# Optimization experiments

Hardware: AMD Instinct MI355X
Metric: run time of the kernel (lower is better)

Reference implementation:

```python
import jax, jax.numpy as jnp
import numpy as np
import math

N_LAYERS = 2
N_HEADS = 8
D_MODEL = 512
D_FF = 2048
B = 2
L = 2048
GELU_C = 0.7978845608028654  # sqrt(2/pi)
LN_EPS = 1e-5


def gelu_tanh(x):
    # faithful to the module's custom GELU: 0.5*x*(1+tanh(sqrt(2/pi)*(x+0.044715*x^3)))
    return 0.5 * x * (1.0 + jnp.tanh(GELU_C * (x + 0.044715 * x * x * x)))


def layernorm(x, g, b):
    m = jnp.mean(x, axis=-1, keepdims=True)
    v = jnp.mean((x - m) ** 2, axis=-1, keepdims=True)
    return (x - m) * jax.lax.rsqrt(v + LN_EPS) * g + b


def setup_inputs() -> dict:
    key = jax.random.key(0)
    ks = jax.random.split(key, 24)
    w = lambda k, shape: jax.random.normal(k, shape, dtype=jnp.float32) * 0.02
    inp = {
        "x": jax.random.normal(ks[0], (B, L, D_MODEL), dtype=jnp.float32),
        # tau is exp(tau_learner(...)) in the full model -> positive scalar per batch
        "tau": jax.random.uniform(ks[1], (B, 1), dtype=jnp.float32) + 0.5,
        "delta": jax.random.normal(ks[2], (B, L), dtype=jnp.float32) * 0.1,
        # NStransformer builds an upper-triangular causal mask (True = masked)
        "att_mask": jnp.triu(jnp.ones((L, L), dtype=bool), k=1),
        "Wq": w(ks[3], (N_LAYERS, D_MODEL, D_MODEL)), "bq": jnp.zeros((N_LAYERS, D_MODEL), jnp.float32),
        "Wk": w(ks[4], (N_LAYERS, D_MODEL, D_MODEL)), "bk": jnp.zeros((N_LAYERS, D_MODEL), jnp.float32),
        "Wv": w(ks[5], (N_LAYERS, D_MODEL, D_MODEL)), "bv": jnp.zeros((N_LAYERS, D_MODEL), jnp.float32),
        "Wo": w(ks[6], (N_LAYERS, D_MODEL, D_MODEL)), "bo": jnp.zeros((N_LAYERS, D_MODEL), jnp.float32),
        # conv1/conv2 are kernel_size=1 Conv1d == pointwise linears
        "W1": w(ks[7], (N_LAYERS, D_MODEL, D_FF)), "b1": jnp.zeros((N_LAYERS, D_FF), jnp.float32),
        "W2": w(ks[8], (N_LAYERS, D_FF, D_MODEL)), "b2": jnp.zeros((N_LAYERS, D_MODEL), jnp.float32),
        "ln1_g": jnp.ones((N_LAYERS, D_MODEL), jnp.float32), "ln1_b": jnp.zeros((N_LAYERS, D_MODEL), jnp.float32),
        "ln2_g": jnp.ones((N_LAYERS, D_MODEL), jnp.float32), "ln2_b": jnp.zeros((N_LAYERS, D_MODEL), jnp.float32),
        "lnf_g": jnp.ones((D_MODEL,), jnp.float32), "lnf_b": jnp.zeros((D_MODEL,), jnp.float32),
    }
    return inp


def reference(x, tau, delta, att_mask, Wq, bq, Wk, bk, Wv, bv, Wo, bo,
              W1, b1, W2, b2, ln1_g, ln1_b, ln2_g, ln2_b, lnf_g, lnf_b):
    Bsz, Ls, D = x.shape
    H = N_HEADS
    E = D // H
    scale = 1.0 / math.sqrt(E)
    t = tau[:, None, None, :]    # (B,1) -> (B,1,1,1)
    d = delta[:, None, None, :]  # (B,L) -> (B,1,1,L)
    neg_inf = jnp.float32(-jnp.inf)
    for l in range(N_LAYERS):
        q = (x @ Wq[l] + bq[l]).reshape(Bsz, Ls, H, E)
        k = (x @ Wk[l] + bk[l]).reshape(Bsz, Ls, H, E)
        v = (x @ Wv[l] + bv[l]).reshape(Bsz, Ls, H, E)
        # de-stationary scores: QK^T * tau + delta, then masked softmax
        scores = jnp.einsum('blhe,bshe->bhls', q, k) * t + d  # (B,H,L,S)
        scores = jnp.where(att_mask, neg_inf, scores)
        A = jax.nn.softmax(scale * scores, axis=-1)  # dropout is identity in eval
        V = jnp.einsum('bhls,bshd->blhd', A, v).reshape(Bsz, Ls, D)
        x = (V @ Wo[l] + bo[l]) + x
        xb = layernorm(x, ln1_g[l], ln1_b[l])
        h = gelu_tanh(xb @ W1[l] + b1[l])   # conv1 (k=1)
        o = h @ W2[l] + b2[l]               # conv2 (k=1)
        x = layernorm(o + xb, ln2_g[l], ln2_b[l])
    return layernorm(x, lnf_g, lnf_b)
```

## Files before the change

### kernel.cpp

```cpp
#include <hip/hip_runtime.h>
#include <stdint.h>

#define DM   512
#define DFF  2048
#define NH   8
#define EH   64
#define SEQ  2048
#define NBAT 2
#define NTOK (NBAT*SEQ)
#define LOG2E 1.44269504088896340736f

typedef __attribute__((ext_vector_type(8))) short  s16x8;
typedef __attribute__((ext_vector_type(8))) __bf16 bf16x8;
typedef __attribute__((ext_vector_type(4))) float  f32x4;

__device__ __forceinline__ short f2bf(float f) {
  union { float f; unsigned int i; } c; c.f = f;
  unsigned int x = c.i;
  x += 0x7fffu + ((x >> 16) & 1u);
  return (short)(x >> 16);
}
__device__ __forceinline__ float bf2f(short u) {
  union { unsigned int i; float f; } c;
  c.i = ((unsigned int)(unsigned short)u) << 16;
  return c.f;
}
__device__ __forceinline__ f32x4 mfma16(bf16x8 a, bf16x8 b, f32x4 c) {
  return __builtin_amdgcn_mfma_f32_16x16x32_bf16(a, b, c, 0, 0, 0);
}
__device__ __forceinline__ void gl_lds16(const short* g, short* l) {
  __builtin_amdgcn_global_load_lds(
      (const __attribute__((address_space(1))) unsigned int*)(const void*)g,
      (__attribute__((address_space(3))) unsigned int*)(void*)l, 16, 0, 0);
}

__global__ __launch_bounds__(256) void fill_code_f32(float* __restrict__ out,
                                                     float code)
{
  out[blockIdx.x * 256 + threadIdx.x] = code;
}

__global__ __launch_bounds__(256) void prep_all(
    const float* __restrict__ Wq, const float* __restrict__ Wk,
    const float* __restrict__ Wv, const float* __restrict__ Wo,
    const float* __restrict__ W1, const float* __restrict__ W2,
    short* __restrict__ Wqkvt, short* __restrict__ Wot,
    short* __restrict__ W1t,   short* __restrict__ W2t,
    const float* __restrict__ x, float* __restrict__ sumf,
    short* __restrict__ x16)
{
  if (blockIdx.x >= 3072) {
    int i = (blockIdx.x - 3072) * 256 + threadIdx.x;
    float v = x[i];
    sumf[i] = v;
    x16[i]  = f2bf(v);
    return;
  }
  int gw   = blockIdx.x * 4 + (threadIdx.x >> 6);
  int lane = threadIdx.x & 63;
  int l = gw / 6144;
  int g = gw % 6144;
  const float* src; short* dst; int K, N, gi;
  if (g < 2048) {
    int w = g >> 9; gi = g & 511; K = 512; N = 512;
    src = (w == 0 ? Wq : w == 1 ? Wk : w == 2 ? Wv : Wo) + l * 262144;
    dst = (w < 3) ? (Wqkvt + l * 786432 + w * 262144) : (Wot + l * 262144);
  } else if (g < 4096) {
    gi = g - 2048; K = 512; N = 2048;
    src = W1 + l * 1048576; dst = W1t + l * 1048576;
  } else {
    gi = g - 4096; K = 2048; N = 512;
    src = W2 + l * 1048576; dst = W2t + l * 1048576;
  }
  int nb = N >> 6;
  int n  = (gi % nb) * 64 + lane;
  int k0 = (gi / nb) * 8;
  s16x8 v;
  #pragma unroll
  for (int i = 0; i < 8; i++) v[i] = f2bf(src[(size_t)(k0 + i) * N + n]);
  *(s16x8*)(dst + (size_t)n * K + k0) = v;
}

__global__ __launch_bounds__(256) void skred_ln(
    const short* __restrict__ parts, const float* __restrict__ bias,
    const float* __restrict__ rf, const short* __restrict__ rb,
    const float* __restrict__ g, const float* __restrict__ bb,
    float* __restrict__ sumf, short* __restrict__ outb, int mode)
{
  const int row  = blockIdx.x * 4 + (threadIdx.x >> 6);
  const int lane = threadIdx.x & 63;
  const int col  = lane * 8;
  const size_t base = (size_t)row * DM + col;
  float t[8];
  #pragma unroll
  for (int j = 0; j < 8; j++) t[j] = bias[col + j];
  #pragma unroll
  for (int p = 0; p < 4; p++) {
    s16x8 v = *(const s16x8*)(parts + (size_t)p * (NTOK * DM) + base);
    #pragma unroll
    for (int j = 0; j < 8; j++) t[j] += bf2f(v[j]);
  }
  if (mode == 0) {
    #pragma unroll
    for (int j = 0; j < 8; j++) t[j] += rf[base + j];
  } else {
    s16x8 v = *(const s16x8*)(rb + base);
    #pragma unroll
    for (int j = 0; j < 8; j++) t[j] += bf2f(v[j]);
  }
  float s = 0.f, ss = 0.f;
  #pragma unroll
  for (int j = 0; j < 8; j++) { s += t[j]; ss += t[j] * t[j]; }
  #pragma unroll
  for (int off = 32; off > 0; off >>= 1) {
    s += __shfl_xor(s, off); ss += __shfl_xor(ss, off);
  }
  float mean = s * (1.f / DM);
  float var  = ss * (1.f / DM) - mean * mean;
  float rstd = rsqrtf(var + 1e-5f);
  if (mode == 0) {
    #pragma unroll
    for (int j = 0; j < 8; j++) {
      sumf[base + j] = t[j];
      outb[base + j] = f2bf((t[j] - mean) * rstd * g[col + j] + bb[col + j]);
    }
  } else {
    #pragma unroll
    for (int j = 0; j < 8; j++) {
      float y = (t[j] - mean) * rstd * g[col + j] + bb[col + j];
      sumf[base + j] = y;
      outb[base + j] = f2bf(y);
    }
  }
}

template<int TM>
__global__ __launch_bounds__(256) void gemm_bt(
    const short* __restrict__ A, const short* __restrict__ Bt,
    int M, int N, int K, int KS, int mode,
    const float* __restrict__ bq, const float* __restrict__ bk,
    const float* __restrict__ bv,
    short* __restrict__ oq, short* __restrict__ okk, short* __restrict__ ov)
{
  __shared__ short As[2][2][TM * 32];
  __shared__ short Bs[2][2][128 * 32];
  constexpr int MT = TM / 32;
  const int tid  = threadIdx.x;
  const int lane = tid & 63;
  const int wid  = tid >> 6;
  const int lm   = lane & 15, quad = lane >> 4;
  const int nbn  = N >> 7;
  const int nb2  = (M / TM) * nbn;
  const int ks   = blockIdx.x / nb2;
  const int rem  = blockIdx.x % nb2;
  const int m0   = (rem / nbn) * TM;
  const int n0   = (rem % nbn) << 7;
  const int wm   = (wid & 1) * (TM / 2), wn = (wid >> 1) * 64;
  const int Kc   = K / KS;
  const int kbeg = ks * Kc;

  f32x4 acc[MT][4];
  #pragma unroll
  for (int i = 0; i < MT; i++)
    #pragma unroll
    for (int j = 0; j < 4; j++) acc[i][j] = (f32x4){0.f, 0.f, 0.f, 0.f};

  const short* Abase = A  + (size_t)m0 * K;
  const short* Bbase = Bt + (size_t)n0 * K;

  auto stage = [&](int b_, int k0) {
    #pragma unroll
    for (int half = 0; half < 2; half++) {
      const int kk = k0 + half * 32;
      #pragma unroll
      for (int j = 0; j < TM / 64; j++) {
        int c = j * 256 + wid * 64 + lane;
        gl_lds16(Abase + (size_t)(c >> 2) * K + kk + (c & 3) * 8,
                 &As[b_][half][(j * 256 + wid * 64) * 8]);
      }
      #pragma unroll
      for (int j = 0; j < 2; j++) {
        int c = j * 256 + wid * 64 + lane;
        gl_lds16(Bbase + (size_t)(c >> 2) * K + kk + (c & 3) * 8,
                 &Bs[b_][half][(j * 256 + wid * 64) * 8]);
      }
    }
  };

  stage(0, kbeg);
  int buf = 0;
  for (int k0 = kbeg; k0 < kbeg + Kc; k0 += 64) {
    __syncthreads();
    if (k0 + 64 < kbeg + Kc) stage(buf ^ 1, k0 + 64);
    #pragma unroll
    for (int half = 0; half < 2; half++) {
      bf16x8 af[MT], bfr[4];
      #pragma unroll
      for (int t = 0; t < MT; t++)
        af[t] = *(const bf16x8*)
            &As[buf][half][(wm + t * 16 + lm) * 32 + quad * 8];
      #pragma unroll
      for (int t = 0; t < 4; t++)
        bfr[t] = *(const bf16x8*)
            &Bs[buf][half][(wn + t * 16 + lm) * 32 + quad * 8];
      #pragma unroll
      for (int mt = 0; mt < MT; mt++)
        #pragma unroll
        for (int nt = 0; nt < 4; nt++)
          acc[mt][nt] = mfma16(af[mt], bfr[nt], acc[mt][nt]);
    }
    buf ^= 1;
  }

  #pragma unroll
  for (int mt = 0; mt < MT; mt++) {
    int row = m0 + wm + mt * 16 + quad * 4;
    #pragma unroll
    for (int nt = 0; nt < 4; nt++) {
      int col = n0 + wn + nt * 16 + lm;
      f32x4 v = acc[mt][nt];
      if (mode == 0) {
        int which = col >> 9; int d = col & 511;
        int hh = d >> 6; int e = d & 63;
        const float* bias = which == 0 ? bq : which == 1 ? bk : bv;
        float bb = bias[d];
        #pragma unroll
        for (int r = 0; r < 4; r++) {
          int tok = row + r; int bI = tok >> 11, li = tok & 2047;
          float val = v[r] + bb;
          if (which == 0)
            oq [(((size_t)bI * NH + hh) * SEQ + li) * EH + e] = f2bf(val);
          else if (which == 1)
            okk[(((size_t)bI * NH + hh) * SEQ + li) * EH + e] = f2bf(val);
          else
            ov [(((size_t)bI * NH + hh) * EH + e) * SEQ + li] = f2bf(val);
        }
      } else if (mode == 2) {
        float bb = bq[col];
        #pragma unroll
        for (int r = 0; r < 4; r++) {
          float x = v[r] + bb;
          float u = 0.7978845608f * (x + 0.044715f * x * x * x);
          float t = 1.f - 2.f / (1.f + __expf(2.f * u));
          size_t idx = (size_t)(row + r) * N + col;
          oq[idx] = f2bf(0.5f * x * (1.f + t));
        }
      } else {
        short* op = oq + (size_t)ks * M * N;
        #pragma unroll
        for (int r = 0; r < 4; r++)
          op[(size_t)(row + r) * N + col] = f2bf(v[r]);
      }
    }
  }
}

__global__ __launch_bounds__(256) void attn_v7(
    const short* __restrict__ Q, const short* __restrict__ Kg,
    const short* __restrict__ Vt,
    const float* __restrict__ tau, const float* __restrict__ delta,
    short* __restrict__ opart, float* __restrict__ lpart)
{
  __shared__ short Ks[64 * 72];
  __shared__ short Vs[64 * 72];
  __shared__ short Ps[4][16 * 72];
  const int tid  = threadIdx.x;
  const int lane = tid & 63, wid = tid >> 6;
  const int lm = lane & 15, quad = lane >> 4;
  const int t    = blockIdx.x >> 2;
  const int part = blockIdx.x & 3;
  const int qb = 31 - (t & 31);
  const int h  = (t >> 5) & 7;
  const int b  = t >> 8;
  const int q0 = qb * 64;
  const int qw = q0 + wid * 16;
  const size_t bhq = ((size_t)b * NH + h) * SEQ;
  const short* kbase = Kg + bhq * EH;
  const short* vbase = Vt + ((size_t)b * NH + h) * (size_t)(EH * SEQ);

  const int nblk = qb + 1;
  const int kb0 = (nblk * part) >> 2;
  const int kb1 = (nblk * (part + 1)) >> 2;

  bf16x8 qf0 = *(const bf16x8*)(Q + (bhq + qw + lm) * EH + quad * 8);
  bf16x8 qf1 = *(const bf16x8*)(Q + (bhq + qw + lm) * EH + 32 + quad * 8);

  const float st2 = 0.125f * LOG2E * tau[b];
  f32x4 O[4];
  #pragma unroll
  for (int i = 0; i < 4; i++) O[i] = (f32x4){0.f, 0.f, 0.f, 0.f};
  float lr[4] = {0.f, 0.f, 0.f, 0.f};

  const int c0 = tid, c1 = tid + 256;
  const int r0 = c0 >> 3, ch0 = (c0 & 7) * 8;
  const int r1 = c1 >> 3, ch1 = (c1 & 7) * 8;

  for (int kb = kb0; kb < kb1; kb++) {
    const int s0 = kb << 6;
    s16x8 ka = *(const s16x8*)(kbase + (size_t)(s0 + r0) * EH + ch0);
    s16x8 kb_ = *(const s16x8*)(kbase + (size_t)(s0 + r1) * EH + ch1);
    s16x8 va = *(const s16x8*)(vbase + (size_t)r0 * SEQ + s0 + ch0);
    s16x8 vb = *(const s16x8*)(vbase + (size_t)r1 * SEQ + s0 + ch1);
    __syncthreads();
    *(s16x8*)&Ks[r0 * 72 + ch0] = ka;
    *(s16x8*)&Ks[r1 * 72 + ch1] = kb_;
    *(s16x8*)&Vs[r0 * 72 + ch0] = va;
    *(s16x8*)&Vs[r1 * 72 + ch1] = vb;
    __syncthreads();

    f32x4 S[4];
    #pragma unroll
    for (int nt = 0; nt < 4; nt++) {
      S[nt] = (f32x4){0.f, 0.f, 0.f, 0.f};
      S[nt] = mfma16(qf0, *(const bf16x8*)&Ks[(nt*16 + lm) * 72 + quad * 8], S[nt]);
      S[nt] = mfma16(qf1, *(const bf16x8*)&Ks[(nt*16 + lm) * 72 + 32 + quad * 8], S[nt]);
    }
    float dl[4];
    #pragma unroll
    for (int nt = 0; nt < 4; nt++)
      dl[nt] = fmaf(0.125f * LOG2E, delta[(size_t)b * SEQ + s0 + nt * 16 + lm],
                    -8.f);

    const bool diag = (kb == qb);
    #pragma unroll
    for (int r = 0; r < 4; r++) {
      float sc[4];
      #pragma unroll
      for (int nt = 0; nt < 4; nt++) sc[nt] = fmaf(st2, S[nt][r], dl[nt]);
      if (diag) {
        int rowq = qw + quad * 4 + r;
        #pragma unroll
        for (int nt = 0; nt < 4; nt++)
          if (s0 + nt * 16 + lm > rowq) sc[nt] = -__builtin_inff();
      }
      unsigned int u0 = __float_as_uint(exp2f(sc[0]));
      unsigned int u1 = __float_as_uint(exp2f(sc[1]));
      unsigned int u2 = __float_as_uint(exp2f(sc[2]));
      unsigned int u3 = __float_as_uint(exp2f(sc[3]));
      lr[r] += (__uint_as_float(u0 & 0xffff0000u) +
                __uint_as_float(u1 & 0xffff0000u)) +
               (__uint_as_float(u2 & 0xffff0000u) +
                __uint_as_float(u3 & 0xffff0000u));
      short* pr = &Ps[wid][(quad * 4 + r) * 72];
      pr[lm]      = (short)(u0 >> 16);
      pr[16 + lm] = (short)(u1 >> 16);
      pr[32 + lm] = (short)(u2 >> 16);
      pr[48 + lm] = (short)(u3 >> 16);
    }

    bf16x8 pf0 = *(const bf16x8*)&Ps[wid][lm * 72 + quad * 8];
    bf16x8 pf1 = *(const bf16x8*)&Ps[wid][lm * 72 + 32 + quad * 8];
    #pragma unroll
    for (int et = 0; et < 4; et++) {
      O[et] = mfma16(pf0, *(const bf16x8*)&Vs[(et*16 + lm) * 72 + quad * 8], O[et]);
      O[et] = mfma16(pf1, *(const bf16x8*)&Vs[(et*16 + lm) * 72 + 32 + quad * 8], O[et]);
    }
  }

  #pragma unroll
  for (int r = 0; r < 4; r++) {
    float s = lr[r];
    #pragma unroll
    for (int off = 1; off < 16; off <<= 1) s += __shfl_xor(s, off);
    lr[r] = s;
  }

  const int slot = ((t << 2) | part);
  short* ob = opart + (size_t)slot * 4096;
  float* lb = lpart + (size_t)slot * 64;
  #pragma unroll
  for (int r = 0; r < 4; r++) {
    int qloc = wid * 16 + quad * 4 + r;
    #pragma unroll
    for (int et = 0; et < 4; et++)
      ob[qloc * 64 + et * 16 + lm] = f2bf(O[et][r]);
    if (lm == 0) lb[qloc] = lr[r];
  }
}

__global__ __launch_bounds__(256) void attn_reduce(
    const short* __restrict__ opart, const float* __restrict__ lpart,
    short* __restrict__ Oa)
{
  const int t = blockIdx.x;
  const int qb = 31 - (t & 31);
  const int h  = (t >> 5) & 7;
  const int b  = t >> 8;
  const int q0 = qb * 64;
  #pragma unroll
  for (int i = 0; i < 16; i++) {
    int idx = i * 256 + threadIdx.x;
    int q = idx >> 6, e = idx & 63;
    float l = 0.f, o = 0.f;
    #pragma unroll
    for (int p = 0; p < 4; p++) {
      int slot = t * 4 + p;
      l += lpart[(size_t)slot * 64 + q];
      o += bf2f(opart[(size_t)slot * 4096 + idx]);
    }
    Oa[((size_t)b * SEQ + q0 + q) * DM + h * EH + e] = f2bf(o / l);
  }
}

__global__ __launch_bounds__(256) void ln_kernel(
    const float* in, const float* __restrict__ g, const float* __restrict__ bb,
    float* outf, short* outb)
{
  int row  = blockIdx.x * 4 + (threadIdx.x >> 6);
  int lane = threadIdx.x & 63;
  const float* p = in + (size_t)row * DM;
  float v[8]; float s = 0.f, ss = 0.f;
  #pragma unroll
  for (int i = 0; i < 8; i++) {
    float x = p[lane + i * 64]; v[i] = x; s += x; ss += x * x;
  }
  #pragma unroll
  for (int off = 32; off > 0; off >>= 1) {
    s += __shfl_xor(s, off); ss += __shfl_xor(ss, off);
  }
  float mean = s * (1.f / DM);
  float var  = ss * (1.f / DM) - mean * mean;
  float rstd = rsqrtf(var + 1e-5f);
  #pragma unroll
  for (int i = 0; i < 8; i++) {
    int c = lane + i * 64;
    float y = (v[i] - mean) * rstd * g[c] + bb[c];
    if (outf) outf[(size_t)row * DM + c] = y;
    if (outb) outb[(size_t)row * DM + c] = f2bf(y);
  }
}

extern "C" void kernel_launch(void* const* d_in, const int* in_sizes, int n_in,
                              void* d_out, int out_size, void* d_ws, size_t ws_size,
                              hipStream_t stream)
{
  float* out = (float*)d_out;

  if (ws_size < (size_t)62918656) {
    fill_code_f32<<<2097152 / 256, 256, 0, stream>>>(
        out, 1200.f + (float)(ws_size >> 20));
    return;
  }

  const float* x    = (const float*)d_in[0];
  const float* tau  = (const float*)d_in[1];
  const float* del  = (const float*)d_in[2];
  const float* Wq = (const float*)d_in[4];
  const float* bq = (const float*)d_in[5];
  const float* Wk = (const float*)d_in[6];
  const float* bk = (const float*)d_in[7];
  const float* Wv = (const float*)d_in[8];
  const float* bv = (const float*)d_in[9];
  const float* Wo = (const float*)d_in[10];
  const float* bo = (const float*)d_in[11];
  const float* W1 = (const float*)d_in[12];
  const float* b1 = (const float*)d_in[13];
  const float* W2 = (const float*)d_in[14];
  const float* b2 = (const float*)d_in[15];
  const float* ln1g = (const float*)d_in[16];
  const float* ln1b = (const float*)d_in[17];
  const float* ln2g = (const float*)d_in[18];
  const float* ln2b = (const float*)d_in[19];
  const float* lnfg = (const float*)d_in[20];
  const float* lnfb = (const float*)d_in[21];

  char* ws = (char*)d_ws;
  float* sumf  = (float*)(ws + 0);
  short* x16   = (short*)(ws + 8388608);
  short* xb16  = (short*)(ws + 12582912);
  short* q16   = (short*)(ws + 16777216);
  short* k16   = (short*)(ws + 20971520);
  short* vt16  = (short*)(ws + 25165824);
  short* at16  = (short*)(ws + 29360128);
  short* h16   = (short*)(ws + 33554432);
  short* Wqkvt = (short*)(ws + 50331648);
  short* Wot   = (short*)(ws + 53477376);
  short* W1t   = (short*)(ws + 54525952);
  short* W2t   = (short*)(ws + 58720256);
  short* aopart = (short*)(ws + 33554432);
  float* alpart = (float*)(ws + 12582912);
  short* oppart = (short*)(ws + 33554432);
  short* f2part = (short*)(ws + 16777216);

  prep_all<<<11264, 256, 0, stream>>>(Wq, Wk, Wv, Wo, W1, W2,
                                      Wqkvt, Wot, W1t, W2t, x, sumf, x16);

  for (int l = 0; l < 2; l++) {
    gemm_bt<64><<<64 * 12, 256, 0, stream>>>(x16, Wqkvt + l * 786432,
        NTOK, 3 * DM, DM, 1, 0,
        bq + l * DM, bk + l * DM, bv + l * DM,
        q16, k16, vt16);
    attn_v7<<<4 * NBAT * NH * (SEQ / 64), 256, 0, stream>>>(
        q16, k16, vt16, tau, del, aopart, alpart);
    attn_reduce<<<NBAT * NH * (SEQ / 64), 256, 0, stream>>>(
        aopart, alpart, at16);
    gemm_bt<64><<<64 * 4 * 4, 256, 0, stream>>>(at16, Wot + l * 262144,
        NTOK, DM, DM, 4, 4,
        nullptr, nullptr, nullptr,
        oppart, nullptr, nullptr);
    skred_ln<<<1024, 256, 0, stream>>>(oppart, bo + l * DM, sumf, nullptr,
        ln1g + l * DM, ln1b + l * DM, sumf, xb16, 0);
    gemm_bt<64><<<64 * 16, 256, 0, stream>>>(xb16, W1t + l * 1048576,
        NTOK, DFF, DM, 1, 2,
        b1 + l * DFF, nullptr, nullptr,
        h16, nullptr, nullptr);
    gemm_bt<64><<<64 * 4 * 4, 256, 0, stream>>>(h16, W2t + l * 1048576,
        NTOK, DM, DFF, 4, 4,
        nullptr, nullptr, nullptr,
        f2part, nullptr, nullptr);
    skred_ln<<<1024, 256, 0, stream>>>(f2part, b2 + l * DM, nullptr, xb16,
        ln2g + l * DM, ln2b + l * DM, sumf, x16, 1);
  }
  ln_kernel<<<NTOK / 4, 256, 0, stream>>>(sumf, lnfg, lnfb, out, nullptr);
}
```

Measured before the change: 410.9 us.

## Fuse final layernorm into last skred_ln, single-buffer GEMM, reorder attention blocks

The final layernorm is folded into the last layer's residual+LN kernel through a new mode 2, which drops one launch and one fp32 round trip of the activations. The GEMM loses its LDS double buffering and now loads and then syncs on every K-step. That cuts shared memory use but exposes global load latency. Attention blocks are re-indexed so that batch/head varies fastest, which changes scheduling order and may help cache locality for K/V.

```diff
diff --git a/kernel.cpp b/kernel.cpp
--- a/kernel.cpp
+++ b/kernel.cpp
@@ -85,7 +85,9 @@
     const short* __restrict__ parts, const float* __restrict__ bias,
     const float* __restrict__ rf, const short* __restrict__ rb,
     const float* __restrict__ g, const float* __restrict__ bb,
-    float* __restrict__ sumf, short* __restrict__ outb, int mode)
+    const float* __restrict__ g2, const float* __restrict__ bb2,
+    float* __restrict__ sumf, short* __restrict__ outb,
+    float* __restrict__ outf32, int mode)
 {
   const int row  = blockIdx.x * 4 + (threadIdx.x >> 6);
   const int lane = threadIdx.x & 63;
@@ -124,13 +126,30 @@
       sumf[base + j] = t[j];
       outb[base + j] = f2bf((t[j] - mean) * rstd * g[col + j] + bb[col + j]);
     }
-  } else {
+  } else if (mode == 1) {
     #pragma unroll
     for (int j = 0; j < 8; j++) {
       float y = (t[j] - mean) * rstd * g[col + j] + bb[col + j];
       sumf[base + j] = y;
       outb[base + j] = f2bf(y);
     }
+  } else {
+    float y[8]; float s2 = 0.f, ss2 = 0.f;
+    #pragma unroll
+    for (int j = 0; j < 8; j++) {
+      y[j] = (t[j] - mean) * rstd * g[col + j] + bb[col + j];
+      s2 += y[j]; ss2 += y[j] * y[j];
+    }
+    #pragma unroll
+    for (int off = 32; off > 0; off >>= 1) {
+      s2 += __shfl_xor(s2, off); ss2 += __shfl_xor(ss2, off);
+    }
+    float mean2 = s2 * (1.f / DM);
+    float var2  = ss2 * (1.f / DM) - mean2 * mean2;
+    float rstd2 = rsqrtf(var2 + 1e-5f);
+    #pragma unroll
+    for (int j = 0; j < 8; j++)
+      outf32[base + j] = (y[j] - mean2) * rstd2 * g2[col + j] + bb2[col + j];
   }
 }
 
@@ -142,8 +161,8 @@
     const float* __restrict__ bv,
     short* __restrict__ oq, short* __restrict__ okk, short* __restrict__ ov)
 {
-  __shared__ short As[2][2][TM * 32];
-  __shared__ short Bs[2][2][128 * 32];
+  __shared__ short As[2][TM * 32];
+  __shared__ short Bs[2][128 * 32];
   constexpr int MT = TM / 32;
   const int tid  = threadIdx.x;
   const int lane = tid & 63;
@@ -168,7 +187,8 @@
   const short* Abase = A  + (size_t)m0 * K;
   const short* Bbase = Bt + (size_t)n0 * K;
 
-  auto stage = [&](int b_, int k0) {
+  for (int k0 = kbeg; k0 < kbeg + Kc; k0 += 64) {
+    __syncthreads();
     #pragma unroll
     for (int half = 0; half < 2; half++) {
       const int kk = k0 + half * 32;
@@ -176,40 +196,31 @@
       for (int j = 0; j < TM / 64; j++) {
         int c = j * 256 + wid * 64 + lane;
         gl_lds16(Abase + (size_t)(c >> 2) * K + kk + (c & 3) * 8,
-                 &As[b_][half][(j * 256 + wid * 64) * 8]);
+                 &As[half][(j * 256 + wid * 64) * 8]);
       }
       #pragma unroll
       for (int j = 0; j < 2; j++) {
         int c = j * 256 + wid * 64 + lane;
         gl_lds16(Bbase + (size_t)(c >> 2) * K + kk + (c & 3) * 8,
-                 &Bs[b_][half][(j * 256 + wid * 64) * 8]);
+                 &Bs[half][(j * 256 + wid * 64) * 8]);
       }
     }
-  };
-
-  stage(0, kbeg);
-  int buf = 0;
-  for (int k0 = kbeg; k0 < kbeg + Kc; k0 += 64) {
     __syncthreads();
-    if (k0 + 64 < kbeg + Kc) stage(buf ^ 1, k0 + 64);
     #pragma unroll
     for (int half = 0; half < 2; half++) {
       bf16x8 af[MT], bfr[4];
       #pragma unroll
       for (int t = 0; t < MT; t++)
-        af[t] = *(const bf16x8*)
-            &As[buf][half][(wm + t * 16 + lm) * 32 + quad * 8];
+        af[t] = *(const bf16x8*)&As[half][(wm + t * 16 + lm) * 32 + quad * 8];
       #pragma unroll
       for (int t = 0; t < 4; t++)
-        bfr[t] = *(const bf16x8*)
-            &Bs[buf][half][(wn + t * 16 + lm) * 32 + quad * 8];
+        bfr[t] = *(const bf16x8*)&Bs[half][(wn + t * 16 + lm) * 32 + quad * 8];
       #pragma unroll
       for (int mt = 0; mt < MT; mt++)
         #pragma unroll
         for (int nt = 0; nt < 4; nt++)
           acc[mt][nt] = mfma16(af[mt], bfr[nt], acc[mt][nt]);
     }
-    buf ^= 1;
   }
 
   #pragma unroll
@@ -267,16 +278,20 @@
   const int tid  = threadIdx.x;
   const int lane = tid & 63, wid = tid >> 6;
   const int lm = lane & 15, quad = lane >> 4;
-  const int t    = blockIdx.x >> 2;
-  const int part = blockIdx.x & 3;
-  const int qb = 31 - (t & 31);
-  const int h  = (t >> 5) & 7;
-  const int b  = t >> 8;
+  const int blk   = blockIdx.x;
+  const int bh    = blk & 15;
+  const int rest  = blk >> 4;
+  const int part  = rest & 3;
+  const int qbrev = rest >> 2;
+  const int qb = 31 - qbrev;
+  const int h  = bh & 7;
+  const int b  = bh >> 3;
   const int q0 = qb * 64;
   const int qw = q0 + wid * 16;
-  const size_t bhq = ((size_t)b * NH + h) * SEQ;
+  const int t_lin = bh * 32 + qbrev;
+  const size_t bhq = (size_t)bh * SEQ;
   const short* kbase = Kg + bhq * EH;
-  const short* vbase = Vt + ((size_t)b * NH + h) * (size_t)(EH * SEQ);
+  const short* vbase = Vt + (size_t)bh * (EH * SEQ);
 
   const int nblk = qb + 1;
   const int kb0 = (nblk * part) >> 2;
@@ -291,16 +306,15 @@
   for (int i = 0; i < 4; i++) O[i] = (f32x4){0.f, 0.f, 0.f, 0.f};
   float lr[4] = {0.f, 0.f, 0.f, 0.f};
 
-  const int c0 = tid, c1 = tid + 256;
-  const int r0 = c0 >> 3, ch0 = (c0 & 7) * 8;
-  const int r1 = c1 >> 3, ch1 = (c1 & 7) * 8;
+  const int r0 = tid >> 3,         ch0 = (tid & 7) * 8;
+  const int r1 = (tid + 256) >> 3, ch1 = (tid & 7) * 8;
 
   for (int kb = kb0; kb < kb1; kb++) {
     const int s0 = kb << 6;
-    s16x8 ka = *(const s16x8*)(kbase + (size_t)(s0 + r0) * EH + ch0);
+    s16x8 ka  = *(const s16x8*)(kbase + (size_t)(s0 + r0) * EH + ch0);
     s16x8 kb_ = *(const s16x8*)(kbase + (size_t)(s0 + r1) * EH + ch1);
-    s16x8 va = *(const s16x8*)(vbase + (size_t)r0 * SEQ + s0 + ch0);
-    s16x8 vb = *(const s16x8*)(vbase + (size_t)r1 * SEQ + s0 + ch1);
+    s16x8 va  = *(const s16x8*)(vbase + (size_t)r0 * SEQ + s0 + ch0);
+    s16x8 vb  = *(const s16x8*)(vbase + (size_t)r1 * SEQ + s0 + ch1);
     __syncthreads();
     *(s16x8*)&Ks[r0 * 72 + ch0] = ka;
     *(s16x8*)&Ks[r1 * 72 + ch1] = kb_;
@@ -365,7 +379,7 @@
     lr[r] = s;
   }
 
-  const int slot = ((t << 2) | part);
+  const int slot = ((t_lin << 2) | part);
   short* ob = opart + (size_t)slot * 4096;
   float* lb = lpart + (size_t)slot * 64;
   #pragma unroll
@@ -399,34 +413,6 @@
       o += bf2f(opart[(size_t)slot * 4096 + idx]);
     }
     Oa[((size_t)b * SEQ + q0 + q) * DM + h * EH + e] = f2bf(o / l);
-  }
-}
-
-__global__ __launch_bounds__(256) void ln_kernel(
-    const float* in, const float* __restrict__ g, const float* __restrict__ bb,
-    float* outf, short* outb)
-{
-  int row  = blockIdx.x * 4 + (threadIdx.x >> 6);
-  int lane = threadIdx.x & 63;
-  const float* p = in + (size_t)row * DM;
-  float v[8]; float s = 0.f, ss = 0.f;
-  #pragma unroll
-  for (int i = 0; i < 8; i++) {
-    float x = p[lane + i * 64]; v[i] = x; s += x; ss += x * x;
-  }
-  #pragma unroll
-  for (int off = 32; off > 0; off >>= 1) {
-    s += __shfl_xor(s, off); ss += __shfl_xor(ss, off);
-  }
-  float mean = s * (1.f / DM);
-  float var  = ss * (1.f / DM) - mean * mean;
-  float rstd = rsqrtf(var + 1e-5f);
-  #pragma unroll
-  for (int i = 0; i < 8; i++) {
-    int c = lane + i * 64;
-    float y = (v[i] - mean) * rstd * g[c] + bb[c];
-    if (outf) outf[(size_t)row * DM + c] = y;
-    if (outb) outb[(size_t)row * DM + c] = f2bf(y);
   }
 }
 
@@ -499,7 +485,8 @@
         nullptr, nullptr, nullptr,
         oppart, nullptr, nullptr);
     skred_ln<<<1024, 256, 0, stream>>>(oppart, bo + l * DM, sumf, nullptr,
-        ln1g + l * DM, ln1b + l * DM, sumf, xb16, 0);
+        ln1g + l * DM, ln1b + l * DM, nullptr, nullptr,
+        sumf, xb16, nullptr, 0);
     gemm_bt<64><<<64 * 16, 256, 0, stream>>>(xb16, W1t + l * 1048576,
         NTOK, DFF, DM, 1, 2,
         b1 + l * DFF, nullptr, nullptr,
@@ -508,8 +495,14 @@
         NTOK, DM, DFF, 4, 4,
         nullptr, nullptr, nullptr,
         f2part, nullptr, nullptr);
-    skred_ln<<<1024, 256, 0, stream>>>(f2part, b2 + l * DM, nullptr, xb16,
-        ln2g + l * DM, ln2b + l * DM, sumf, x16, 1);
-  }
-  ln_kernel<<<NTOK / 4, 256, 0, stream>>>(sumf, lnfg, lnfb, out, nullptr);
-}
+    if (l == 0) {
+      skred_ln<<<1024, 256, 0, stream>>>(f2part, b2 + l * DM, nullptr, xb16,
+          ln2g + l * DM, ln2b + l * DM, nullptr, nullptr,
+          sumf, x16, nullptr, 1);
+    } else {
+      skred_ln<<<1024, 256, 0, stream>>>(f2part, b2 + l * DM, nullptr, xb16,
+          ln2g + l * DM, ln2b + l * DM, lnfg, lnfb,
+          nullptr, nullptr, out, 2);
+    }
+  }
+}
```

Result: faster. 383.4 us (-6.7%).
